# Optimization experiments

Measured on AMD Instinct MI355X. Metric: run time of the kernel, lower is better.

Reference implementation:

```python
import jax, jax.numpy as jnp
import numpy as np

B, IN, OUT = 131072, 256, 256
BITWIDTH = 7.0


def setup_inputs() -> dict:
    key = jax.random.key(0)
    k1, k2 = jax.random.split(key)
    # simulated int8 activations (integer-valued float32)
    act_in = jax.random.randint(k1, (B, IN), -127, 128).astype(jnp.float32)
    # UniformWeights: xavier_uniform then weight_quant to the int8 grid
    limit = float(np.sqrt(6.0 / (IN + OUT)))
    w = jax.random.uniform(k2, (OUT, IN), minval=-limit, maxval=limit, dtype=jnp.float32)
    w_range = jnp.max(jnp.abs(w))
    weight_exp = (jnp.ceil(jnp.log2(w_range)) - 7.0).astype(jnp.int32)
    weight = jnp.round(w / w_range * 127.0)  # int8-valued float32 [OUT, IN]
    return {"act_in": act_in, "exp_in": jnp.int32(0), "weight": weight, "weight_exp": weight_exp}


def _round_shift(x, shift):
    # RoundShift: floor-div by 2**shift, add floor(|remainder| / 2**(shift-1)), clip to int8
    two_s = jnp.exp2(shift)
    rt = jnp.floor(x / two_s)
    prob = jnp.abs(x - rt * two_s)
    dec = jnp.floor(prob / jnp.exp2(shift - 1.0))
    return jnp.clip(rt + dec, -127.0, 127.0)


def reference(act_in, exp_in, weight, weight_exp):
    # int8 GEMM simulated in fp32 (exact: |acc| < 2^24)
    temp = act_in @ weight.T  # [B, OUT] int32 accumulator values
    # RangeEstimate: full-tensor abs-max -> bitwidth
    r = jnp.max(jnp.abs(temp))
    bw = jnp.where(r > 0, jnp.ceil(jnp.log2(jnp.maximum(r, 1.0))), 0.0)
    shift = bw - BITWIDTH
    pos = shift > 0
    safe_shift = jnp.maximum(shift, 1.0)
    rounded = _round_shift(temp, safe_shift)
    act_out = jnp.where(pos, rounded, temp).astype(jnp.int8)
    exp_sum = jnp.asarray(exp_in, jnp.int32) + jnp.asarray(weight_exp, jnp.int32)
    exp_out = (exp_sum + jnp.where(pos, shift, 0.0).astype(jnp.int32)).astype(jnp.int16)
    return act_out, exp_out
```

## Files before the change

### kernel.cpp

```cpp
#include <hip/hip_runtime.h>
#include <stdint.h>


#define M_ROWS 131072
#define NK 256
#define TM 128
#define TILES 4
#define LSTR 272

typedef __attribute__((ext_vector_type(4))) int iv4;
typedef __attribute__((ext_vector_type(4))) float fv4;
typedef __attribute__((ext_vector_type(4))) unsigned int u32x4;

__device__ __forceinline__ iv4 mfma_i8(iv4 a, iv4 b, iv4 c) {
  asm("v_mfma_i32_16x16x64_i8 %0, %1, %2, %0" : "+v"(c) : "v"(a), "v"(b));
  return c;
}

__device__ __forceinline__ unsigned int pack_i8x4(float a, float b, float c,
                                                  float d) {
  return ((unsigned int)(int)a & 0xFFu) | (((unsigned int)(int)b & 0xFFu) << 8) |
         (((unsigned int)(int)c & 0xFFu) << 16) | ((unsigned int)(int)d << 24);
}

__global__ void wconv(const float* __restrict__ w, unsigned char* __restrict__ wi8,
                      int* __restrict__ gmax) {
  if (blockIdx.x == 0 && threadIdx.x == 0) *gmax = 0;
  const int i = blockIdx.x * 256 + threadIdx.x;
  const fv4 f = ((const fv4*)w)[i];
  ((unsigned int*)wi8)[i] = pack_i8x4(f.x, f.y, f.z, f.w);
}

__global__ __launch_bounds__(512, 1) void gemm_max_cvt(
    const float* __restrict__ act, const unsigned char* __restrict__ wi8,
    unsigned char* __restrict__ act8, int* __restrict__ gmax)
{
  __shared__ __align__(16) unsigned char As[TM * LSTR];
  __shared__ __align__(16) unsigned char Bs[NK * LSTR];
  __shared__ int smax;
  const int tid = threadIdx.x;
  if (tid == 0) smax = 0;

  for (int c = tid; c < NK * NK / 16; c += 512) {
    const int col = c >> 4, kc = (c & 15) << 4;
    *(u32x4*)&Bs[col * LSTR + kc] = *(const u32x4*)(wi8 + col * NK + kc);
  }

  const int lane = tid & 63;
  const int wave = tid >> 6;
  const int wr   = wave >> 2;
  const int wc   = wave & 3;
  const int lm   = lane & 15;
  const int lk   = lane >> 4;

  int imax = 0;

  for (int t = 0; t < TILES; ++t) {
    const int tb = blockIdx.x * (TILES * TM) + t * TM;

    __syncthreads();
#pragma unroll
    for (int j = 0; j < 4; ++j) {
      const int c   = j * 512 + tid;
      const int row = c >> 4;
      const int kc  = (c & 15) << 4;
      const float* p = act + (size_t)(tb + row) * NK + kc;
      const fv4 f0 = ((const fv4*)p)[0];
      const fv4 f1 = ((const fv4*)p)[1];
      const fv4 f2 = ((const fv4*)p)[2];
      const fv4 f3 = ((const fv4*)p)[3];
      u32x4 v;
      v.x = pack_i8x4(f0.x, f0.y, f0.z, f0.w);
      v.y = pack_i8x4(f1.x, f1.y, f1.z, f1.w);
      v.z = pack_i8x4(f2.x, f2.y, f2.z, f2.w);
      v.w = pack_i8x4(f3.x, f3.y, f3.z, f3.w);
      *(u32x4*)&As[row * LSTR + kc] = v;
      *(u32x4*)(act8 + (size_t)(tb + row) * NK + kc) = v;
    }
    __syncthreads();

    iv4 acc[4][4] = {};
#pragma unroll
    for (int kk = 0; kk < 4; ++kk) {
      iv4 af[4], bf[4];
#pragma unroll
      for (int mi = 0; mi < 4; ++mi)
        af[mi] = *(const iv4*)&As[(wr * 64 + mi * 16 + lm) * LSTR + kk * 64 + lk * 16];
#pragma unroll
      for (int ni = 0; ni < 4; ++ni)
        bf[ni] = *(const iv4*)&Bs[(wc * 64 + ni * 16 + lm) * LSTR + kk * 64 + lk * 16];
#pragma unroll
      for (int mi = 0; mi < 4; ++mi)
#pragma unroll
        for (int ni = 0; ni < 4; ++ni)
          acc[mi][ni] = mfma_i8(af[mi], bf[ni], acc[mi][ni]);
    }

#pragma unroll
    for (int mi = 0; mi < 4; ++mi)
#pragma unroll
      for (int ni = 0; ni < 4; ++ni)
#pragma unroll
        for (int r = 0; r < 4; ++r) {
          const int ti = acc[mi][ni][r];
          const int a = ti < 0 ? -ti : ti;
          imax = a > imax ? a : imax;
        }
  }

#pragma unroll
  for (int off = 32; off; off >>= 1) {
    const int o = __shfl_xor(imax, off, 64);
    imax = o > imax ? o : imax;
  }
  if (lane == 0) atomicMax(&smax, imax);
  __syncthreads();
  if (tid == 0) atomicMax(gmax, smax);
}

__global__ __launch_bounds__(512, 2) void gemm_quant(
    const unsigned char* __restrict__ act8, const unsigned char* __restrict__ wi8,
    int* __restrict__ out, const int* __restrict__ gmax,
    const int* __restrict__ exp_in, const int* __restrict__ wexp)
{
  __shared__ __align__(16) unsigned char Bs[NK * LSTR];

  const int rmax = *gmax;
  const int bw = (rmax <= 1) ? 0 : (32 - __clz(rmax - 1));
  const int shift = bw - 7;
  const bool pos = shift > 0;
  const int s = shift < 1 ? 1 : shift;

  const int tid = threadIdx.x;
  for (int c = tid; c < NK * NK / 16; c += 512) {
    const int col = c >> 4, kc = (c & 15) << 4;
    *(u32x4*)&Bs[col * LSTR + kc] = *(const u32x4*)(wi8 + (size_t)col * NK + kc);
  }
  __syncthreads();

  const int lane = tid & 63;
  const int wave = tid >> 6;
  const int wr   = wave >> 2;
  const int wc   = wave & 3;
  const int lm   = lane & 15;
  const int lk   = lane >> 4;
  const int tb   = blockIdx.x * TM;

  const unsigned char* arow = act8 + (size_t)(tb + wr * 64 + lm) * NK + lk * 16;

  iv4 acc[4][4] = {};
#pragma unroll
  for (int kk = 0; kk < 4; ++kk) {
    iv4 af[4], bf[4];
#pragma unroll
    for (int mi = 0; mi < 4; ++mi)
      af[mi] = *(const iv4*)(arow + (size_t)(mi * 16) * NK + kk * 64);
#pragma unroll
    for (int ni = 0; ni < 4; ++ni)
      bf[ni] = *(const iv4*)&Bs[(wc * 64 + ni * 16 + lm) * LSTR + kk * 64 + lk * 16];
#pragma unroll
    for (int mi = 0; mi < 4; ++mi)
#pragma unroll
      for (int ni = 0; ni < 4; ++ni)
        acc[mi][ni] = mfma_i8(af[mi], bf[ni], acc[mi][ni]);
  }

#pragma unroll
  for (int mi = 0; mi < 4; ++mi)
#pragma unroll
    for (int ni = 0; ni < 4; ++ni)
#pragma unroll
      for (int r = 0; r < 4; ++r) {
        const int ti = acc[mi][ni][r];
        int q;
        if (pos) {
          const int rt = ti >> s;
          const int dec = (ti - (rt << s)) >> (s - 1);
          q = rt + dec;
          q = q > 127 ? 127 : (q < -127 ? -127 : q);
        } else {
          q = (int)(signed char)(ti & 0xFF);
        }
        const int m = tb + wr * 64 + mi * 16 + lk * 4 + r;
        const int n = wc * 64 + ni * 16 + lm;
        __builtin_nontemporal_store(q, &out[(size_t)m * NK + n]);
      }

  if (blockIdx.x == 0 && tid == 0) {
    const int e = exp_in[0] + wexp[0] + (pos ? shift : 0);
    out[(size_t)M_ROWS * NK] = (int)(short)e;
  }
}

extern "C" void kernel_launch(void* const* d_in, const int* in_sizes, int n_in,
                              void* d_out, int out_size, void* d_ws, size_t ws_size,
                              hipStream_t stream) {
  const float* act   = (const float*)d_in[0];
  const int* exp_in  = (const int*)d_in[1];
  const float* wgt   = (const float*)d_in[2];
  const int* wexp    = (const int*)d_in[3];
  int* gmax           = (int*)d_ws;
  unsigned char* wi8  = (unsigned char*)d_ws + 4096;
  unsigned char* act8 = (unsigned char*)d_ws + (1 << 20);

  wconv<<<dim3(64), dim3(256), 0, stream>>>(wgt, wi8, gmax);
  gemm_max_cvt<<<dim3(M_ROWS / (TILES * TM)), dim3(512), 0, stream>>>(
      act, wi8, act8, gmax);
  gemm_quant<<<dim3(M_ROWS / TM), dim3(512), 0, stream>>>(act8, wi8, (int*)d_out,
                                                          gmax, exp_in, wexp);
}
```

Before: 271.7 us.

## Fuse GEMM passes into one cooperative kernel with grid sync, keeping activations in LDS

Merges the max-finding GEMM and the quantizing GEMM into one cooperative kernel. Each block converts 512 rows of activations to int8 in LDS once, computes the GEMM for the global abs-max, waits on a grid-wide sync, then recomputes the GEMM from LDS and writes quantized outputs. This removes the int8 activation round trip through global memory and one kernel launch. In exchange, weight fragments are now read straight from global memory or cache instead of LDS, and the 256 blocks must all be co-resident for the grid sync (144KB LDS per block), which may limit occupancy.

```diff
diff --git a/kernel.cpp b/kernel.cpp
--- a/kernel.cpp
+++ b/kernel.cpp
@@ -1,12 +1,14 @@
 #include <hip/hip_runtime.h>
+#include <hip/hip_cooperative_groups.h>
 #include <stdint.h>
+
+namespace cg = cooperative_groups;
 
 
 #define M_ROWS 131072
 #define NK 256
-#define TM 128
-#define TILES 4
-#define LSTR 272
+#define BLK_ROWS 512
+#define ASTR 288
 
 typedef __attribute__((ext_vector_type(4))) int iv4;
 typedef __attribute__((ext_vector_type(4))) float fv4;
@@ -31,73 +33,64 @@
   ((unsigned int*)wi8)[i] = pack_i8x4(f.x, f.y, f.z, f.w);
 }
 
-__global__ __launch_bounds__(512, 1) void gemm_max_cvt(
+__global__ __launch_bounds__(1024, 4) void fused(
     const float* __restrict__ act, const unsigned char* __restrict__ wi8,
-    unsigned char* __restrict__ act8, int* __restrict__ gmax)
+    int* __restrict__ out, int* __restrict__ gmax,
+    const int* __restrict__ exp_in, const int* __restrict__ wexp)
 {
-  __shared__ __align__(16) unsigned char As[TM * LSTR];
-  __shared__ __align__(16) unsigned char Bs[NK * LSTR];
+  __shared__ __align__(16) unsigned char As[BLK_ROWS * ASTR];
   __shared__ int smax;
   const int tid = threadIdx.x;
   if (tid == 0) smax = 0;
 
-  for (int c = tid; c < NK * NK / 16; c += 512) {
-    const int col = c >> 4, kc = (c & 15) << 4;
-    *(u32x4*)&Bs[col * LSTR + kc] = *(const u32x4*)(wi8 + col * NK + kc);
+  const size_t rowbase = (size_t)blockIdx.x * BLK_ROWS;
+
+#pragma unroll 2
+  for (int it = 0; it < 8; ++it) {
+    const int c   = it * 1024 + tid;
+    const int row = c >> 4;
+    const int kc  = (c & 15) << 4;
+    const float* p = act + (rowbase + row) * NK + kc;
+    const fv4 f0 = ((const fv4*)p)[0];
+    const fv4 f1 = ((const fv4*)p)[1];
+    const fv4 f2 = ((const fv4*)p)[2];
+    const fv4 f3 = ((const fv4*)p)[3];
+    u32x4 v;
+    v.x = pack_i8x4(f0.x, f0.y, f0.z, f0.w);
+    v.y = pack_i8x4(f1.x, f1.y, f1.z, f1.w);
+    v.z = pack_i8x4(f2.x, f2.y, f2.z, f2.w);
+    v.w = pack_i8x4(f3.x, f3.y, f3.z, f3.w);
+    *(u32x4*)&As[row * ASTR + kc] = v;
   }
+  __syncthreads();
 
   const int lane = tid & 63;
-  const int wave = tid >> 6;
-  const int wr   = wave >> 2;
-  const int wc   = wave & 3;
+  const int w    = tid >> 6;
   const int lm   = lane & 15;
   const int lk   = lane >> 4;
 
   int imax = 0;
-
-  for (int t = 0; t < TILES; ++t) {
-    const int tb = blockIdx.x * (TILES * TM) + t * TM;
-
-    __syncthreads();
 #pragma unroll
-    for (int j = 0; j < 4; ++j) {
-      const int c   = j * 512 + tid;
-      const int row = c >> 4;
-      const int kc  = (c & 15) << 4;
-      const float* p = act + (size_t)(tb + row) * NK + kc;
-      const fv4 f0 = ((const fv4*)p)[0];
-      const fv4 f1 = ((const fv4*)p)[1];
-      const fv4 f2 = ((const fv4*)p)[2];
-      const fv4 f3 = ((const fv4*)p)[3];
-      u32x4 v;
-      v.x = pack_i8x4(f0.x, f0.y, f0.z, f0.w);
-      v.y = pack_i8x4(f1.x, f1.y, f1.z, f1.w);
-      v.z = pack_i8x4(f2.x, f2.y, f2.z, f2.w);
-      v.w = pack_i8x4(f3.x, f3.y, f3.z, f3.w);
-      *(u32x4*)&As[row * LSTR + kc] = v;
-      *(u32x4*)(act8 + (size_t)(tb + row) * NK + kc) = v;
-    }
-    __syncthreads();
-
-    iv4 acc[4][4] = {};
+  for (int ni4 = 0; ni4 < 4; ++ni4) {
+    iv4 acc[2][4] = {};
 #pragma unroll
     for (int kk = 0; kk < 4; ++kk) {
-      iv4 af[4], bf[4];
+      iv4 af[2], bf[4];
 #pragma unroll
-      for (int mi = 0; mi < 4; ++mi)
-        af[mi] = *(const iv4*)&As[(wr * 64 + mi * 16 + lm) * LSTR + kk * 64 + lk * 16];
+      for (int mi = 0; mi < 2; ++mi)
+        af[mi] = *(const iv4*)&As[(w * 32 + mi * 16 + lm) * ASTR + kk * 64 + lk * 16];
 #pragma unroll
       for (int ni = 0; ni < 4; ++ni)
-        bf[ni] = *(const iv4*)&Bs[(wc * 64 + ni * 16 + lm) * LSTR + kk * 64 + lk * 16];
+        bf[ni] = *(const iv4*)(wi8 +
+            (size_t)(ni4 * 64 + ni * 16 + lm) * NK + kk * 64 + lk * 16);
 #pragma unroll
-      for (int mi = 0; mi < 4; ++mi)
+      for (int mi = 0; mi < 2; ++mi)
 #pragma unroll
         for (int ni = 0; ni < 4; ++ni)
           acc[mi][ni] = mfma_i8(af[mi], bf[ni], acc[mi][ni]);
     }
-
 #pragma unroll
-    for (int mi = 0; mi < 4; ++mi)
+    for (int mi = 0; mi < 2; ++mi)
 #pragma unroll
       for (int ni = 0; ni < 4; ++ni)
 #pragma unroll
@@ -107,7 +100,6 @@
           imax = a > imax ? a : imax;
         }
   }
-
 #pragma unroll
   for (int off = 32; off; off >>= 1) {
     const int o = __shfl_xor(imax, off, 64);
@@ -116,75 +108,57 @@
   if (lane == 0) atomicMax(&smax, imax);
   __syncthreads();
   if (tid == 0) atomicMax(gmax, smax);
-}
+  __threadfence();
 
-__global__ __launch_bounds__(512, 2) void gemm_quant(
-    const unsigned char* __restrict__ act8, const unsigned char* __restrict__ wi8,
-    int* __restrict__ out, const int* __restrict__ gmax,
-    const int* __restrict__ exp_in, const int* __restrict__ wexp)
-{
-  __shared__ __align__(16) unsigned char Bs[NK * LSTR];
+  cg::this_grid().sync();
 
-  const int rmax = *gmax;
+  const int rmax = __hip_atomic_load(gmax, __ATOMIC_RELAXED,
+                                     __HIP_MEMORY_SCOPE_AGENT);
   const int bw = (rmax <= 1) ? 0 : (32 - __clz(rmax - 1));
   const int shift = bw - 7;
   const bool pos = shift > 0;
   const int s = shift < 1 ? 1 : shift;
 
-  const int tid = threadIdx.x;
-  for (int c = tid; c < NK * NK / 16; c += 512) {
-    const int col = c >> 4, kc = (c & 15) << 4;
-    *(u32x4*)&Bs[col * LSTR + kc] = *(const u32x4*)(wi8 + (size_t)col * NK + kc);
-  }
-  __syncthreads();
-
-  const int lane = tid & 63;
-  const int wave = tid >> 6;
-  const int wr   = wave >> 2;
-  const int wc   = wave & 3;
-  const int lm   = lane & 15;
-  const int lk   = lane >> 4;
-  const int tb   = blockIdx.x * TM;
-
-  const unsigned char* arow = act8 + (size_t)(tb + wr * 64 + lm) * NK + lk * 16;
-
-  iv4 acc[4][4] = {};
 #pragma unroll
-  for (int kk = 0; kk < 4; ++kk) {
-    iv4 af[4], bf[4];
+  for (int ni4 = 0; ni4 < 4; ++ni4) {
+    iv4 acc[2][4] = {};
 #pragma unroll
-    for (int mi = 0; mi < 4; ++mi)
-      af[mi] = *(const iv4*)(arow + (size_t)(mi * 16) * NK + kk * 64);
+    for (int kk = 0; kk < 4; ++kk) {
+      iv4 af[2], bf[4];
 #pragma unroll
-    for (int ni = 0; ni < 4; ++ni)
-      bf[ni] = *(const iv4*)&Bs[(wc * 64 + ni * 16 + lm) * LSTR + kk * 64 + lk * 16];
-#pragma unroll
-    for (int mi = 0; mi < 4; ++mi)
+      for (int mi = 0; mi < 2; ++mi)
+        af[mi] = *(const iv4*)&As[(w * 32 + mi * 16 + lm) * ASTR + kk * 64 + lk * 16];
 #pragma unroll
       for (int ni = 0; ni < 4; ++ni)
-        acc[mi][ni] = mfma_i8(af[mi], bf[ni], acc[mi][ni]);
+        bf[ni] = *(const iv4*)(wi8 +
+            (size_t)(ni4 * 64 + ni * 16 + lm) * NK + kk * 64 + lk * 16);
+#pragma unroll
+      for (int mi = 0; mi < 2; ++mi)
+#pragma unroll
+        for (int ni = 0; ni < 4; ++ni)
+          acc[mi][ni] = mfma_i8(af[mi], bf[ni], acc[mi][ni]);
+    }
+#pragma unroll
+    for (int mi = 0; mi < 2; ++mi)
+#pragma unroll
+      for (int ni = 0; ni < 4; ++ni)
+#pragma unroll
+        for (int r = 0; r < 4; ++r) {
+          const int ti = acc[mi][ni][r];
+          int q;
+          if (pos) {
+            const int rt = ti >> s;
+            const int dec = (ti - (rt << s)) >> (s - 1);
+            q = rt + dec;
+            q = q > 127 ? 127 : (q < -127 ? -127 : q);
+          } else {
+            q = (int)(signed char)(ti & 0xFF);
+          }
+          const size_t m = rowbase + w * 32 + mi * 16 + lk * 4 + r;
+          const int n = ni4 * 64 + ni * 16 + lm;
+          __builtin_nontemporal_store(q, &out[m * NK + n]);
+        }
   }
-
-#pragma unroll
-  for (int mi = 0; mi < 4; ++mi)
-#pragma unroll
-    for (int ni = 0; ni < 4; ++ni)
-#pragma unroll
-      for (int r = 0; r < 4; ++r) {
-        const int ti = acc[mi][ni][r];
-        int q;
-        if (pos) {
-          const int rt = ti >> s;
-          const int dec = (ti - (rt << s)) >> (s - 1);
-          q = rt + dec;
-          q = q > 127 ? 127 : (q < -127 ? -127 : q);
-        } else {
-          q = (int)(signed char)(ti & 0xFF);
-        }
-        const int m = tb + wr * 64 + mi * 16 + lk * 4 + r;
-        const int n = wc * 64 + ni * 16 + lm;
-        __builtin_nontemporal_store(q, &out[(size_t)m * NK + n]);
-      }
 
   if (blockIdx.x == 0 && tid == 0) {
     const int e = exp_in[0] + wexp[0] + (pos ? shift : 0);
@@ -201,11 +175,12 @@
   const int* wexp    = (const int*)d_in[3];
   int* gmax           = (int*)d_ws;
   unsigned char* wi8  = (unsigned char*)d_ws + 4096;
-  unsigned char* act8 = (unsigned char*)d_ws + (1 << 20);
 
   wconv<<<dim3(64), dim3(256), 0, stream>>>(wgt, wi8, gmax);
-  gemm_max_cvt<<<dim3(M_ROWS / (TILES * TM)), dim3(512), 0, stream>>>(
-      act, wi8, act8, gmax);
-  gemm_quant<<<dim3(M_ROWS / TM), dim3(512), 0, stream>>>(act8, wi8, (int*)d_out,
-                                                          gmax, exp_in, wexp);
+
+  int* outp = (int*)d_out;
+  void* args[] = {(void*)&act, (void*)&wi8, (void*)&outp,
+                  (void*)&gmax, (void*)&exp_in, (void*)&wexp};
+  (void)hipLaunchCooperativeKernel((void*)fused, dim3(M_ROWS / BLK_ROWS),
+                                   dim3(1024), args, 0, stream);
 }
```

After: 396.1 us. 1.46x slower.
